# Performance work log

Measured on AMD Instinct MI355X. Metric: run time of the kernel, lower is better.

The kernel has to match this reference:

```python
import jax, jax.numpy as jnp
import numpy as np

# Elliptical structuring-element sizes (cv2.MORPH_ELLIPSE-like), per init_kwargs.
KERNEL_SIZES = [3, 5, 7]
B, C, H, W = 16, 1, 1024, 1024
_MAX_VAL = 1e4  # kornia's max_val; geodesic border padding uses +-max_val
_EPS = 1e-7     # smp DiceLoss eps


def _ellipse_offsets(k):
    """Offsets (i, j) within a k x k window where the elliptical mask is 1."""
    r = k // 2
    yy, xx = np.mgrid[-r:r + 1, -r:r + 1]
    rr = max(r, 1)
    mask = (xx / rr) ** 2 + (yy / rr) ** 2 <= 1.0 + 1e-9
    return [(i, j) for i in range(k) for j in range(k) if mask[i, j]]


def _morph(x, k, offsets, is_dilation):
    """Flat morphological dilation (max) / erosion (min) over the ellipse support.
    Matches kornia's unfold-based morphology with geodesic border handling,
    but computed as a fused running max/min over static shifted views (no unfold blow-up)."""
    pad = k // 2
    fill = -_MAX_VAL if is_dilation else _MAX_VAL
    xp = jnp.pad(x, ((0, 0), (0, 0), (pad, pad), (pad, pad)), constant_values=fill)
    h, w = x.shape[-2], x.shape[-1]
    op = jnp.maximum if is_dilation else jnp.minimum
    i0, j0 = offsets[0]
    out = xp[..., i0:i0 + h, j0:j0 + w]
    for (i, j) in offsets[1:]:
        out = op(out, xp[..., i:i + h, j:j + w])
    return out


def _dice_loss(pred, target):
    """smp.losses.DiceLoss(mode='binary', from_logits=False): reduce over dims (batch, pixels)."""
    b = pred.shape[0]
    p = pred.reshape(b, 1, -1)
    t = target.reshape(b, 1, -1)
    inter = jnp.sum(p * t, axis=(0, 2))            # [1]
    card = jnp.sum(p + t, axis=(0, 2))             # [1]
    score = 2.0 * inter / jnp.clip(card, _EPS)
    loss = (1.0 - score) * (jnp.sum(t, axis=(0, 2)) > 0)
    return jnp.mean(loss)


def setup_inputs() -> dict:
    key = jax.random.key(0)
    k1, k2 = jax.random.split(key)
    pred = jax.random.uniform(k1, (B, C, H, W), dtype=jnp.float32)
    teacher = jax.random.uniform(k2, (B, C, H, W), dtype=jnp.float32)
    return {"pred_student_prob": pred, "teacher_prob": teacher}


def reference(pred_student_prob, teacher_prob):
    teacher = jax.lax.stop_gradient(teacher_prob)  # .detach()
    total = jnp.float32(0.0)
    for k in KERNEL_SIZES:
        offs = _ellipse_offsets(k)
        obj_dil = _morph(teacher, k, offs, True)
        obj_ero = _morph(teacher, k, offs, False)
        total = total + _dice_loss(pred_student_prob, obj_dil) + _dice_loss(pred_student_prob, obj_ero)
    return total / len(KERNEL_SIZES)
```

## Files before the change

kernel.cpp:

```cpp
#include <hip/hip_runtime.h>

#define H_ 1024
#define W_ 1024
#define B_ 16
#define TH 4
#define STEPS (TH + 6)
#define GX (H_ / TH)
#define NBLK (GX * B_)
#define NACC 13
#define TW 4
#define BT 256


__global__ __launch_bounds__(BT, 2) void k_partials(const float* __restrict__ pred,
                                                    const float* __restrict__ tch,
                                                    float* __restrict__ partials) {
  const int tid = threadIdx.x;
  const int n     = blockIdx.y * gridDim.x + blockIdx.x;
  const int b     = n >> 8;
  const int loc   = n & 255;
  const int ytile = (loc & 7) * 32 + (loc >> 3);
  const int y0    = ytile * TH;
  const int x0    = tid * TW;
  const float* tb = tch  + (size_t)b * (H_ * W_);
  const float* pb = pred + (size_t)b * (H_ * W_);

  float acc[NACC];
#pragma unroll
  for (int j = 0; j < NACC; j++) acc[j] = 0.f;

  float ring[7][12];

#pragma unroll
  for (int s = 0; s < STEPS; ++s) {
    {
      const int t    = y0 + s - 3;
      const int trow = t < 0 ? 0 : (t >= H_ ? H_ - 1 : t);
      const float* tr = tb + (size_t)trow * W_ + x0;
      const float4 v1 = *reinterpret_cast<const float4*>(tr);
      ring[s % 7][4] = v1.x; ring[s % 7][5] = v1.y; ring[s % 7][6] = v1.z; ring[s % 7][7] = v1.w;
      if (tid > 0) {
        const float4 vl = *reinterpret_cast<const float4*>(tr - 4);
        ring[s % 7][0] = vl.x; ring[s % 7][1] = vl.y; ring[s % 7][2] = vl.z; ring[s % 7][3] = vl.w;
      } else {
        ring[s % 7][0] = ring[s % 7][1] = ring[s % 7][2] = ring[s % 7][3] = v1.x;
      }
      if (tid < BT - 1) {
        const float4 vr = *reinterpret_cast<const float4*>(tr + 4);
        ring[s % 7][8] = vr.x; ring[s % 7][9] = vr.y; ring[s % 7][10] = vr.z; ring[s % 7][11] = vr.w;
      } else {
        ring[s % 7][8] = ring[s % 7][9] = ring[s % 7][10] = ring[s % 7][11] = v1.w;
      }
    }

    if (s >= 6) {
      const float (&rm3)[12] = ring[(s + 1) % 7];
      const float (&rm2)[12] = ring[(s + 2) % 7];
      const float (&rm1)[12] = ring[(s + 3) % 7];
      const float (&rc )[12] = ring[(s + 4) % 7];
      const float (&rp1)[12] = ring[(s + 5) % 7];
      const float (&rp2)[12] = ring[(s + 6) % 7];
      const float (&rp3)[12] = ring[s % 7];

      const float* pr = pb + (size_t)(y0 + s - 6) * W_ + x0;
      const float4 p1 = *reinterpret_cast<const float4*>(pr);
      const float p[TW] = {p1.x, p1.y, p1.z, p1.w};

      {
        float V3[12], V5[12];
#pragma unroll
        for (int i = 2; i <= 9; ++i) {
          V3[i] = fmaxf(fmaxf(rm1[i], rc[i]), rp1[i]);
          V5[i] = fmaxf(fmaxf(V3[i], rm2[i]), rp2[i]);
        }
#pragma unroll
        for (int c = 0; c < TW; ++c) {
          const int i = c + 4;
          const float V7 = fmaxf(fmaxf(V5[i], rm3[i]), rp3[i]);
          const float d3 = fmaxf(fmaxf(V3[i], rc[i - 1]), rc[i + 1]);
          float d5 = fmaxf(fmaxf(V5[i], V3[i - 1]), V3[i + 1]);
          d5 = fmaxf(fmaxf(d5, rc[i - 2]), rc[i + 2]);
          float d7 = fmaxf(fmaxf(V7, V5[i - 1]), V5[i + 1]);
          d7 = fmaxf(fmaxf(d7, V5[i - 2]), V5[i + 2]);
          d7 = fmaxf(fmaxf(d7, rc[i - 3]), rc[i + 3]);
          acc[0]  += p[c];
          acc[1]  += d3;  acc[2]  = fmaf(p[c], d3, acc[2]);
          acc[5]  += d5;  acc[6]  = fmaf(p[c], d5, acc[6]);
          acc[9]  += d7;  acc[10] = fmaf(p[c], d7, acc[10]);
        }
      }
      {
        float V3[12], V5[12];
#pragma unroll
        for (int i = 2; i <= 9; ++i) {
          V3[i] = fminf(fminf(rm1[i], rc[i]), rp1[i]);
          V5[i] = fminf(fminf(V3[i], rm2[i]), rp2[i]);
        }
#pragma unroll
        for (int c = 0; c < TW; ++c) {
          const int i = c + 4;
          const float V7 = fminf(fminf(V5[i], rm3[i]), rp3[i]);
          const float e3 = fminf(fminf(V3[i], rc[i - 1]), rc[i + 1]);
          float e5 = fminf(fminf(V5[i], V3[i - 1]), V3[i + 1]);
          e5 = fminf(fminf(e5, rc[i - 2]), rc[i + 2]);
          float e7 = fminf(fminf(V7, V5[i - 1]), V5[i + 1]);
          e7 = fminf(fminf(e7, V5[i - 2]), V5[i + 2]);
          e7 = fminf(fminf(e7, rc[i - 3]), rc[i + 3]);
          acc[3]  += e3;  acc[4]  = fmaf(p[c], e3, acc[4]);
          acc[7]  += e5;  acc[8]  = fmaf(p[c], e5, acc[8]);
          acc[11] += e7;  acc[12] = fmaf(p[c], e7, acc[12]);
        }
      }
    }
  }

#pragma unroll
  for (int j = 0; j < NACC; j++) {
    float v = acc[j];
#pragma unroll
    for (int off = 32; off > 0; off >>= 1) v += __shfl_down(v, off, 64);
    acc[j] = v;
  }
  __shared__ float red[4][NACC];
  const int lane = tid & 63, wv = tid >> 6;
  if (lane == 0) {
#pragma unroll
    for (int j = 0; j < NACC; j++) red[wv][j] = acc[j];
  }
  __syncthreads();
  if (tid == 0) {
#pragma unroll
    for (int j = 0; j < NACC; j++)
      partials[j * NBLK + n] = red[0][j] + red[1][j] + red[2][j] + red[3][j];
  }
}

__global__ __launch_bounds__(256) void k_final(const float* __restrict__ partials,
                                               float* __restrict__ out) {
  const int tid = threadIdx.x;
  double acc[NACC];
#pragma unroll
  for (int j = 0; j < NACC; j++) acc[j] = 0.0;
#pragma unroll
  for (int k = 0; k < NBLK / 256; k++) {
#pragma unroll
    for (int j = 0; j < NACC; j++)
      acc[j] += (double)partials[j * NBLK + tid + k * 256];
  }
#pragma unroll
  for (int j = 0; j < NACC; j++) {
#pragma unroll
    for (int off = 32; off > 0; off >>= 1) acc[j] += __shfl_down(acc[j], off, 64);
  }
  __shared__ double red[4][NACC];
  const int lane = tid & 63, wv = tid >> 6;
  if (lane == 0) {
#pragma unroll
    for (int j = 0; j < NACC; j++) red[wv][j] = acc[j];
  }
  __syncthreads();
  if (tid == 0) {
    double t_[NACC];
#pragma unroll
    for (int j = 0; j < NACC; j++) t_[j] = red[0][j] + red[1][j] + red[2][j] + red[3][j];
    const double Sp = t_[0];
    double total = 0.0;
#pragma unroll
    for (int k = 0; k < 3; k++) {
      const double Sd = t_[1 + 4 * k], Id = t_[2 + 4 * k];
      const double Se = t_[3 + 4 * k], Ie = t_[4 + 4 * k];
      double cd = Sp + Sd; if (cd < 1e-7) cd = 1e-7;
      double ce = Sp + Se; if (ce < 1e-7) ce = 1e-7;
      total += (1.0 - 2.0 * Id / cd) * (Sd > 0.0 ? 1.0 : 0.0);
      total += (1.0 - 2.0 * Ie / ce) * (Se > 0.0 ? 1.0 : 0.0);
    }
    out[0] = (float)(total / 3.0);
  }
}

extern "C" void kernel_launch(void* const* d_in, const int* in_sizes, int n_in,
                              void* d_out, int out_size, void* d_ws, size_t ws_size,
                              hipStream_t stream) {
  const float* pred = (const float*)d_in[0];
  const float* tch  = (const float*)d_in[1];
  float* partials = (float*)d_ws;

  k_partials<<<dim3(GX, B_), BT, 0, stream>>>(pred, tch, partials);
  k_final<<<1, 256, 0, stream>>>(partials, (float*)d_out);
}
```

Baseline: 157.6 us.

## Replace halo loads with wave shuffles, prefetch pred, raise occupancy, split final reduction

Each thread now loads only its own float4 of every teacher row. The left and right 3-pixel halos come from DPP/shuffle exchanges with neighbouring lanes, and only wave-edge lanes issue extra global loads. This cuts the redundant halo traffic from three float4 loads per row to about one. The pred row is prefetched one step ahead, and launch_bounds asks for 4 blocks per CU instead of 2, which may force tighter register allocation and cause spills. The final reduction is split into a 13-block per-accumulator kernel plus a tiny scalar kernel, which adds one extra kernel launch.

```diff
diff --git a/kernel.cpp b/kernel.cpp
--- a/kernel.cpp
+++ b/kernel.cpp
@@ -12,10 +12,11 @@
 #define BT 256
 
 
-__global__ __launch_bounds__(BT, 2) void k_partials(const float* __restrict__ pred,
+__global__ __launch_bounds__(BT, 4) void k_partials(const float* __restrict__ pred,
                                                     const float* __restrict__ tch,
                                                     float* __restrict__ partials) {
-  const int tid = threadIdx.x;
+  const int tid  = threadIdx.x;
+  const int lane = tid & 63;
   const int n     = blockIdx.y * gridDim.x + blockIdx.x;
   const int b     = n >> 8;
   const int loc   = n & 255;
@@ -29,53 +30,74 @@
 #pragma unroll
   for (int j = 0; j < NACC; j++) acc[j] = 0.f;
 
-  float ring[7][12];
+  float ring[7][10];
+  const float* trp = nullptr;
+  float4 pv, pvn;
 
 #pragma unroll
   for (int s = 0; s < STEPS; ++s) {
+    if (s >= 1) {
+      const int sl = (s - 1) % 7;
+      const float a3 = ring[sl][3], a4 = ring[sl][4], a5 = ring[sl][5], a6 = ring[sl][6];
+      ring[sl][0] = __shfl_up(a4, 1, 64);
+      ring[sl][1] = __shfl_up(a5, 1, 64);
+      ring[sl][2] = __shfl_up(a6, 1, 64);
+      ring[sl][7] = __shfl_down(a3, 1, 64);
+      ring[sl][8] = __shfl_down(a4, 1, 64);
+      ring[sl][9] = __shfl_down(a5, 1, 64);
+      if (lane == 0) {
+        if (tid > 0) {
+          const float4 el = *reinterpret_cast<const float4*>(trp + x0 - 4);
+          ring[sl][0] = el.y; ring[sl][1] = el.z; ring[sl][2] = el.w;
+        } else {
+          ring[sl][0] = ring[sl][1] = ring[sl][2] = a3;
+        }
+      }
+      if (lane == 63) {
+        if (tid < BT - 1) {
+          const float4 er = *reinterpret_cast<const float4*>(trp + x0 + 4);
+          ring[sl][7] = er.x; ring[sl][8] = er.y; ring[sl][9] = er.z;
+        } else {
+          ring[sl][7] = ring[sl][8] = ring[sl][9] = a6;
+        }
+      }
+    }
+
     {
       const int t    = y0 + s - 3;
       const int trow = t < 0 ? 0 : (t >= H_ ? H_ - 1 : t);
-      const float* tr = tb + (size_t)trow * W_ + x0;
-      const float4 v1 = *reinterpret_cast<const float4*>(tr);
-      ring[s % 7][4] = v1.x; ring[s % 7][5] = v1.y; ring[s % 7][6] = v1.z; ring[s % 7][7] = v1.w;
-      if (tid > 0) {
-        const float4 vl = *reinterpret_cast<const float4*>(tr - 4);
-        ring[s % 7][0] = vl.x; ring[s % 7][1] = vl.y; ring[s % 7][2] = vl.z; ring[s % 7][3] = vl.w;
-      } else {
-        ring[s % 7][0] = ring[s % 7][1] = ring[s % 7][2] = ring[s % 7][3] = v1.x;
-      }
-      if (tid < BT - 1) {
-        const float4 vr = *reinterpret_cast<const float4*>(tr + 4);
-        ring[s % 7][8] = vr.x; ring[s % 7][9] = vr.y; ring[s % 7][10] = vr.z; ring[s % 7][11] = vr.w;
-      } else {
-        ring[s % 7][8] = ring[s % 7][9] = ring[s % 7][10] = ring[s % 7][11] = v1.w;
-      }
-    }
+      const float* tr = tb + (size_t)trow * W_;
+      const float4 v  = *reinterpret_cast<const float4*>(tr + x0);
+      const int sl = s % 7;
+      ring[sl][3] = v.x; ring[sl][4] = v.y; ring[sl][5] = v.z; ring[sl][6] = v.w;
+      trp = tr;
+    }
+
+    if (s == 5) pvn = *reinterpret_cast<const float4*>(pb + (size_t)y0 * W_ + x0);
 
     if (s >= 6) {
-      const float (&rm3)[12] = ring[(s + 1) % 7];
-      const float (&rm2)[12] = ring[(s + 2) % 7];
-      const float (&rm1)[12] = ring[(s + 3) % 7];
-      const float (&rc )[12] = ring[(s + 4) % 7];
-      const float (&rp1)[12] = ring[(s + 5) % 7];
-      const float (&rp2)[12] = ring[(s + 6) % 7];
-      const float (&rp3)[12] = ring[s % 7];
-
-      const float* pr = pb + (size_t)(y0 + s - 6) * W_ + x0;
-      const float4 p1 = *reinterpret_cast<const float4*>(pr);
-      const float p[TW] = {p1.x, p1.y, p1.z, p1.w};
+      pv = pvn;
+      if (s < STEPS - 1)
+        pvn = *reinterpret_cast<const float4*>(pb + (size_t)(y0 + s - 5) * W_ + x0);
+      const float (&rm3)[10] = ring[(s - 6) % 7];
+      const float (&rm2)[10] = ring[(s - 5) % 7];
+      const float (&rm1)[10] = ring[(s - 4) % 7];
+      const float (&rc )[10] = ring[(s - 3) % 7];
+      const float (&rp1)[10] = ring[(s - 2) % 7];
+      const float (&rp2)[10] = ring[(s - 1) % 7];
+      const float (&rp3)[10] = ring[s % 7];
+      const float p[TW] = {pv.x, pv.y, pv.z, pv.w};
 
       {
-        float V3[12], V5[12];
-#pragma unroll
-        for (int i = 2; i <= 9; ++i) {
+        float V3[10], V5[10];
+#pragma unroll
+        for (int i = 1; i <= 8; ++i) {
           V3[i] = fmaxf(fmaxf(rm1[i], rc[i]), rp1[i]);
           V5[i] = fmaxf(fmaxf(V3[i], rm2[i]), rp2[i]);
         }
 #pragma unroll
         for (int c = 0; c < TW; ++c) {
-          const int i = c + 4;
+          const int i = c + 3;
           const float V7 = fmaxf(fmaxf(V5[i], rm3[i]), rp3[i]);
           const float d3 = fmaxf(fmaxf(V3[i], rc[i - 1]), rc[i + 1]);
           float d5 = fmaxf(fmaxf(V5[i], V3[i - 1]), V3[i + 1]);
@@ -90,15 +112,15 @@
         }
       }
       {
-        float V3[12], V5[12];
-#pragma unroll
-        for (int i = 2; i <= 9; ++i) {
+        float V3[10], V5[10];
+#pragma unroll
+        for (int i = 1; i <= 8; ++i) {
           V3[i] = fminf(fminf(rm1[i], rc[i]), rp1[i]);
           V5[i] = fminf(fminf(V3[i], rm2[i]), rp2[i]);
         }
 #pragma unroll
         for (int c = 0; c < TW; ++c) {
-          const int i = c + 4;
+          const int i = c + 3;
           const float V7 = fminf(fminf(V5[i], rm3[i]), rp3[i]);
           const float e3 = fminf(fminf(V3[i], rc[i - 1]), rc[i + 1]);
           float e5 = fminf(fminf(V5[i], V3[i - 1]), V3[i + 1]);
@@ -122,7 +144,7 @@
     acc[j] = v;
   }
   __shared__ float red[4][NACC];
-  const int lane = tid & 63, wv = tid >> 6;
+  const int wv = tid >> 6;
   if (lane == 0) {
 #pragma unroll
     for (int j = 0; j < NACC; j++) red[wv][j] = acc[j];
@@ -135,34 +157,28 @@
   }
 }
 
-__global__ __launch_bounds__(256) void k_final(const float* __restrict__ partials,
-                                               float* __restrict__ out) {
+__global__ __launch_bounds__(256) void k_red(const float* __restrict__ partials,
+                                             float* __restrict__ red13) {
+  const int j   = blockIdx.x;
   const int tid = threadIdx.x;
-  double acc[NACC];
-#pragma unroll
-  for (int j = 0; j < NACC; j++) acc[j] = 0.0;
-#pragma unroll
-  for (int k = 0; k < NBLK / 256; k++) {
-#pragma unroll
-    for (int j = 0; j < NACC; j++)
-      acc[j] += (double)partials[j * NBLK + tid + k * 256];
-  }
-#pragma unroll
-  for (int j = 0; j < NACC; j++) {
-#pragma unroll
-    for (int off = 32; off > 0; off >>= 1) acc[j] += __shfl_down(acc[j], off, 64);
-  }
-  __shared__ double red[4][NACC];
+  double a = 0.0;
+#pragma unroll
+  for (int k = 0; k < NBLK / 256; k++)
+    a += (double)partials[j * NBLK + tid + k * 256];
+#pragma unroll
+  for (int off = 32; off > 0; off >>= 1) a += __shfl_down(a, off, 64);
+  __shared__ double red[4];
   const int lane = tid & 63, wv = tid >> 6;
-  if (lane == 0) {
-#pragma unroll
-    for (int j = 0; j < NACC; j++) red[wv][j] = acc[j];
-  }
+  if (lane == 0) red[wv] = a;
   __syncthreads();
-  if (tid == 0) {
+  if (tid == 0) red13[j] = (float)0, red13[j] = (float)(red[0] + red[1] + red[2] + red[3]);
+}
+
+__global__ void k_final(const float* __restrict__ red13, float* __restrict__ out) {
+  if (threadIdx.x == 0) {
     double t_[NACC];
 #pragma unroll
-    for (int j = 0; j < NACC; j++) t_[j] = red[0][j] + red[1][j] + red[2][j] + red[3][j];
+    for (int j = 0; j < NACC; j++) t_[j] = (double)red13[j];
     const double Sp = t_[0];
     double total = 0.0;
 #pragma unroll
@@ -184,7 +200,9 @@
   const float* pred = (const float*)d_in[0];
   const float* tch  = (const float*)d_in[1];
   float* partials = (float*)d_ws;
+  float* red13    = (float*)d_ws + NACC * NBLK;
 
   k_partials<<<dim3(GX, B_), BT, 0, stream>>>(pred, tch, partials);
-  k_final<<<1, 256, 0, stream>>>(partials, (float*)d_out);
-}
+  k_red<<<NACC, 256, 0, stream>>>(partials, red13);
+  k_final<<<1, 64, 0, stream>>>(red13, (float*)d_out);
+}
```

Result: no change. 156.0 us (-1.0%).
